# Performance work log

Measured on AMD Instinct MI355X. Metric: run time of the kernel, lower is better.

The kernel has to match this reference:

```python
import jax, jax.numpy as jnp
import numpy as np

EMB = 1024

def setup_inputs() -> dict:
    key = jax.random.key(0)
    ks = jax.random.split(key, 6)
    B, S, E = 4, 2048, EMB
    x = jax.random.normal(ks[0], (B, S, E), dtype=jnp.float32)
    attention_mask = jax.random.randint(ks[1], (B, S, S), 0, 2, dtype=jnp.int32)
    proj_w = jax.random.normal(ks[2], (E, 3 * E), dtype=jnp.float32) * (1.0 / np.sqrt(E))
    proj_b = jax.random.normal(ks[3], (3 * E,), dtype=jnp.float32) * 0.02
    out_w = jax.random.normal(ks[4], (E, E), dtype=jnp.float32) * (1.0 / np.sqrt(E))
    out_b = jax.random.normal(ks[5], (E,), dtype=jnp.float32) * 0.02
    return {"x": x, "attention_mask": attention_mask, "proj_w": proj_w,
            "proj_b": proj_b, "out_w": out_w, "out_b": out_b}

def reference(x, attention_mask, proj_w, proj_b, out_w, out_b):
    E = x.shape[-1]
    scale = 1.0 / jnp.sqrt(jnp.asarray(E, x.dtype))
    qkv = x @ proj_w + proj_b                      # [B,S,3E]
    q, k, v = jnp.split(qkv, 3, axis=-1)           # each [B,S,E]
    scores = jnp.einsum('bqe,bke->bqk', q, k) * scale  # [B,S,S]
    scores = jnp.where(attention_mask == 0, jnp.asarray(-1e20, scores.dtype), scores)
    attn = jax.nn.softmax(scores, axis=-1)
    ctx = jnp.einsum('bqk,bke->bqe', attn, v)      # [B,S,E]
    return ctx @ out_w + out_b
```

## Files before the change

### kernel.cpp

```cpp
#include <hip/hip_runtime.h>
#include <cstdint>

typedef unsigned short u16;
typedef uint32_t u32;
typedef __bf16 bf16x8 __attribute__((ext_vector_type(8)));
typedef float f32x4 __attribute__((ext_vector_type(4)));

__device__ __forceinline__ u16 f2bf(float f) {
  unsigned u = __float_as_uint(f);
  u += 0x7fffu + ((u >> 16) & 1u);
  return (u16)(u >> 16);
}

__device__ __forceinline__ void async16(const void* g, void* l) {
  __builtin_amdgcn_global_load_lds(
      (const __attribute__((address_space(1))) uint32_t*)g,
      (__attribute__((address_space(3))) uint32_t*)l, 16, 0, 0);
}

__global__ __launch_bounds__(256) void k_prep(const float* __restrict__ x, u16* __restrict__ xb,
                                              const float* __restrict__ pw, u16* __restrict__ wt,
                                              const float* __restrict__ ow, u16* __restrict__ owt,
                                              const int* __restrict__ mask, u32* __restrict__ mbits) {
  const int bid = blockIdx.x;
  if (bid < 8192) {
    const int i = bid * 256 + threadIdx.x;
    const float4 v = ((const float4*)x)[i];
    ushort4 o;
    o.x = f2bf(v.x); o.y = f2bf(v.y); o.z = f2bf(v.z); o.w = f2bf(v.w);
    ((ushort4*)xb)[i] = o;
    return;
  }
  if (bid >= 12288) {
    const size_t w = (size_t)(bid - 12288) * 256 + threadIdx.x;
    const int* p = mask + w * 32;
    u32 bits = 0;
#pragma unroll
    for (int j = 0; j < 8; ++j) {
      const int4 v = ((const int4*)p)[j];
      bits |= (u32)(v.x & 1) << (j * 4 + 0);
      bits |= (u32)(v.y & 1) << (j * 4 + 1);
      bits |= (u32)(v.z & 1) << (j * 4 + 2);
      bits |= (u32)(v.w & 1) << (j * 4 + 3);
    }
    mbits[w] = bits;
    return;
  }
  __shared__ u16 tile[32][33];
  const int tx = threadIdx.x & 31, ty = threadIdx.x >> 5;
  const float* in;
  u16* outp;
  int lda, ldo, c0, r0;
  if (bid < 11264) {
    const int id = bid - 8192;
    c0 = (id % 96) * 32; r0 = (id / 96) * 32;
    in = pw; outp = wt; lda = 3072; ldo = 1024;
  } else {
    const int id = bid - 11264;
    c0 = (id % 32) * 32; r0 = (id / 32) * 32;
    in = ow; outp = owt; lda = 1024; ldo = 1024;
  }
#pragma unroll
  for (int i = 0; i < 4; ++i)
    tile[ty + i * 8][tx] = f2bf(in[(size_t)(r0 + ty + i * 8) * lda + c0 + tx]);
  __syncthreads();
#pragma unroll
  for (int i = 0; i < 4; ++i)
    outp[(size_t)(c0 + ty + i * 8) * ldo + r0 + tx] = tile[tx][ty + i * 8];
}

template <int MODE>
__global__ __launch_bounds__(512, 4) void gemm256(
    const u16* __restrict__ A, long lda, long bsA,
    const u16* __restrict__ Bt, long ldb, long bsB,
    void* __restrict__ C, long ldc, long bsC,
    int M, int N, int K,
    const float* __restrict__ bias, const u32* __restrict__ mbits) {
  __shared__ u16 sm[3][12288];
  const int gx = gridDim.x, gxy = gridDim.x * gridDim.y;
  const int T = gxy * gridDim.z;
  int L = blockIdx.x + gx * blockIdx.y + gxy * blockIdx.z;
  L = (L & 7) * (T >> 3) + (L >> 3);
  const int b = L / gxy, rr = L % gxy, bx = rr % gx, by = rr / gx;
  const int m0 = by * 256, n0 = bx * 128;
  const int tid = threadIdx.x;
  const int lane = tid & 63;
  const int w = tid >> 6;
  const int wr = w >> 1, wc = w & 1;

  const int sl = tid >> 3;
  const int sgo = (tid & 7) ^ (sl & 7);
  const int srow = 2 * sl + (sgo >> 2);
  const int skoff = (sgo & 3) * 8;
  const u16* pa = A + (size_t)b * bsA + (size_t)(m0 + srow) * lda + skoff;
  const u16* pb = Bt + (size_t)b * bsB + (size_t)(n0 + srow) * ldb + skoff;
  const size_t a128 = (size_t)128 * lda;

  const int m_l = lane & 15, q = lane >> 4;
  const int l7 = m_l >> 1;
  const int g = (((m_l & 1) * 4) + q) ^ l7;
  const int aoff = wr * 2048 + l7 * 64 + g * 8;
  const int boff = 8192 + wc * 2048 + l7 * 64 + g * 8;

  f32x4 acc[4][4] = {};

#define MFMA_(A_, B_, C_) __builtin_amdgcn_mfma_f32_16x16x32_bf16(A_, B_, C_, 0, 0, 0)
#define STAGE(tt, bi)                               \
  {                                                 \
    const size_t ko_ = (size_t)(tt)*32;             \
    u16* da_ = &sm[bi][0] + tid * 8;                \
    async16(pa + ko_, da_);                         \
    async16(pa + ko_ + a128, da_ + 4096);           \
    async16(pb + ko_, &sm[bi][8192] + tid * 8);     \
  }

  const int NTL = K >> 5;
  STAGE(0, 0) STAGE(1, 1)
  asm volatile("s_waitcnt vmcnt(3)" ::: "memory");
  asm volatile("s_barrier" ::: "memory");

  int br = 0, bs = 2;
  for (int t = 0; t < NTL; ++t) {
    if (t + 2 < NTL) STAGE(t + 2, bs)
    const u16* ab = &sm[br][0] + aoff;
    const u16* bb = &sm[br][0] + boff;
    bf16x8 af[4], bf[4];
#pragma unroll
    for (int mt = 0; mt < 4; ++mt) af[mt] = *(const bf16x8*)(ab + mt * 512);
#pragma unroll
    for (int nt = 0; nt < 4; ++nt) bf[nt] = *(const bf16x8*)(bb + nt * 512);
    __builtin_amdgcn_s_setprio(1);
#pragma unroll
    for (int mt = 0; mt < 4; ++mt)
#pragma unroll
      for (int nt = 0; nt < 4; ++nt)
        acc[mt][nt] = MFMA_(af[mt], bf[nt], acc[mt][nt]);
    __builtin_amdgcn_s_setprio(0);
    if (t + 2 < NTL) {
      asm volatile("s_waitcnt vmcnt(3)" ::: "memory");
    } else if (t + 1 < NTL) {
      asm volatile("s_waitcnt vmcnt(0)" ::: "memory");
    }
    if (t + 1 < NTL) asm volatile("s_barrier" ::: "memory");
    br = (br == 2) ? 0 : br + 1;
    bs = (bs == 2) ? 0 : bs + 1;
  }
#undef STAGE
#undef MFMA_

  if constexpr (MODE == 1) {
    __syncthreads();
    u32* smw = (u32*)&sm[0][0];
    const int rl = tid >> 1, pr = tid & 1;
    const uint2 mv = *(const uint2*)(mbits + ((size_t)b * M + m0 + rl) * (N >> 5) + (n0 >> 5) + pr * 2);
    smw[rl * 4 + pr * 2] = mv.x;
    smw[rl * 4 + pr * 2 + 1] = mv.y;
    __syncthreads();
  }

#pragma unroll
  for (int mt = 0; mt < 4; ++mt) {
#pragma unroll
    for (int nt = 0; nt < 4; ++nt) {
      const int col = n0 + wc * 64 + nt * 16 + m_l;
      const int row0 = m0 + wr * 64 + mt * 16 + q * 4;
#pragma unroll
      for (int r = 0; r < 4; ++r) {
        const int row = row0 + r;
        float v = acc[mt][nt][r];
        if constexpr (MODE == 0) {
          v += bias[col];
          if (col < 1024) v *= 0.03125f;
          ((u16*)C)[(size_t)b * bsC + (size_t)row * ldc + col] = f2bf(v);
        } else {
          const int cl = wc * 64 + nt * 16 + m_l;
          const int rl2 = wr * 64 + mt * 16 + q * 4 + r;
          const u32 wb = ((const u32*)&sm[0][0])[rl2 * 4 + (cl >> 5)];
          v = ((wb >> (cl & 31)) & 1u) ? __expf(fminf(v, 30.f)) : 0.f;
          ((u16*)C)[(size_t)b * bsC + (size_t)row * ldc + col] = f2bf(v);
        }
      }
    }
  }
}

template <int MODE, int TM, int BN>
__device__ __forceinline__ void gemm_core(
    u16* As, u16* Bs,
    const u16* __restrict__ A, long lda, long bsA,
    const u16* __restrict__ Bt, long ldb, long bsB,
    void* __restrict__ C, long ldc, long bsC,
    int M, int N, int K,
    const float* __restrict__ bias, const u32* __restrict__ mbits,
    int b, int bx, int by) {
  constexpr int MT = TM / 32, NT = BN / 32;
  constexpr int ACALLS = TM / 8, TOT = (TM + BN) / 8, NC = TOT / 4;
  const int m0 = by * TM, n0 = bx * BN;
  const int lane = threadIdx.x & 63;
  const int w = threadIdx.x >> 6;
  const int wr = w >> 1, wc = w & 1;

  const int srow = lane >> 3;
  const int scol = ((lane & 7) ^ ((lane >> 3) & 7)) * 8;
  const u16* pa = A + (size_t)b * bsA + (size_t)(m0 + srow) * lda + scol;
  const u16* pb = Bt + (size_t)b * bsB + (size_t)(n0 + srow) * ldb + scol;

  const int m_l = lane & 15, q = lane >> 4, m7 = m_l & 7;
  const int offs[2] = {(q ^ m7) * 8, ((4 + q) ^ m7) * 8};

  f32x4 acc[MT][NT] = {};
  f32x4 accs[MT] = {};
  bf16x8 ones;
#pragma unroll
  for (int e = 0; e < 8; ++e) ones[e] = (__bf16)1.0f;

  for (int kt = 0; kt < K; kt += 64) {
    __syncthreads();
#pragma unroll
    for (int g = 0; g < NC; ++g) {
      const int idx = w * NC + g;
      if (idx < ACALLS)
        async16(pa + (size_t)(idx * 8) * lda, As + idx * 512);
      else
        async16(pb + (size_t)((idx - ACALLS) * 8) * ldb, Bs + (idx - ACALLS) * 512);
    }
    __syncthreads();
#pragma unroll
    for (int s = 0; s < 2; ++s) {
      bf16x8 af[MT], bfr[NT];
#pragma unroll
      for (int t = 0; t < MT; ++t)
        af[t] = *(const bf16x8*)(As + (wr * (TM / 2) + t * 16 + m_l) * 64 + offs[s]);
#pragma unroll
      for (int t = 0; t < NT; ++t)
        bfr[t] = *(const bf16x8*)(Bs + (wc * (BN / 2) + t * 16 + m_l) * 64 + offs[s]);
#pragma unroll
      for (int mt = 0; mt < MT; ++mt)
#pragma unroll
        for (int nt = 0; nt < NT; ++nt)
          acc[mt][nt] = __builtin_amdgcn_mfma_f32_16x16x32_bf16(af[mt], bfr[nt], acc[mt][nt], 0, 0, 0);
      if constexpr (MODE == 2) {
#pragma unroll
        for (int mt = 0; mt < MT; ++mt)
          accs[mt] = __builtin_amdgcn_mfma_f32_16x16x32_bf16(af[mt], ones, accs[mt], 0, 0, 0);
      }
    }
    pa += 64;
    pb += 64;
  }

  float rinv[MT][4];
  if constexpr (MODE == 2) {
#pragma unroll
    for (int mt = 0; mt < MT; ++mt)
#pragma unroll
      for (int r = 0; r < 4; ++r) rinv[mt][r] = 1.0f / accs[mt][r];
  }

#pragma unroll
  for (int mt = 0; mt < MT; ++mt) {
#pragma unroll
    for (int nt = 0; nt < NT; ++nt) {
      const int col = n0 + wc * (BN / 2) + nt * 16 + m_l;
      const int row0 = m0 + wr * (TM / 2) + mt * 16 + q * 4;
      if constexpr (MODE == 3) {
        ushort4 o;
        o.x = f2bf(acc[mt][nt][0]); o.y = f2bf(acc[mt][nt][1]);
        o.z = f2bf(acc[mt][nt][2]); o.w = f2bf(acc[mt][nt][3]);
        *(ushort4*)((u16*)C + (size_t)b * bsC + (size_t)col * ldc + row0) = o;
      } else {
#pragma unroll
        for (int r = 0; r < 4; ++r) {
          const int row = row0 + r;
          float v = acc[mt][nt][r];
          if constexpr (MODE == 2) {
            v = v * rinv[mt][r] + bias[col];
            ((float*)C)[(size_t)b * bsC + (size_t)row * ldc + col] = v;
          }
        }
      }
    }
  }
}

template <int MODE, int TM, int BN>
__global__ __launch_bounds__(256) void gemm_bt(
    const u16* __restrict__ A, long lda, long bsA,
    const u16* __restrict__ Bt, long ldb, long bsB,
    void* __restrict__ C, long ldc, long bsC,
    int M, int N, int K,
    const float* __restrict__ bias, const u32* __restrict__ mbits) {
  __shared__ u16 As[TM * 64];
  __shared__ u16 Bs[BN * 64];
  const int gx = gridDim.x, gxy = gridDim.x * gridDim.y;
  const int T = gxy * gridDim.z;
  int L = blockIdx.x + gx * blockIdx.y + gxy * blockIdx.z;
  L = (L & 7) * (T >> 3) + (L >> 3);
  const int bz = L / gxy, r = L % gxy;
  gemm_core<MODE, TM, BN>(As, Bs, A, lda, bsA, Bt, ldb, bsB, C, ldc, bsC, M, N, K,
                          bias, mbits, bz, r % gx, r / gx);
}

extern "C" void kernel_launch(void* const* d_in, const int* in_sizes, int n_in,
                              void* d_out, int out_size, void* d_ws, size_t ws_size,
                              hipStream_t stream) {
  const float* x = (const float*)d_in[0];
  const int* mask = (const int*)d_in[1];
  const float* proj_w = (const float*)d_in[2];
  const float* proj_b = (const float*)d_in[3];
  const float* out_w = (const float*)d_in[4];
  const float* out_b = (const float*)d_in[5];
  float* out = (float*)d_out;

  char* ws = (char*)d_ws;
  u16* xb = (u16*)(ws);
  u16* wt = (u16*)(ws + 16777216);
  u16* owt = (u16*)(ws + 23068672);
  u16* qkv = (u16*)(ws + 25165824);
  u16* P = (u16*)(ws + 75497472);
  u32* mbits = (u32*)(ws + 109051904);
  u16* Ut = (u16*)xb;

  k_prep<<<14336, 256, 0, stream>>>(x, xb, proj_w, wt, out_w, owt, mask, mbits);
  gemm256<0><<<dim3(24, 32, 1), 512, 0, stream>>>(
      xb, 1024, 0, wt, 1024, 0, qkv, 3072, 0, 8192, 3072, 1024, proj_b, nullptr);
  gemm256<1><<<dim3(16, 8, 4), 512, 0, stream>>>(
      qkv, 3072, (long)2048 * 3072, qkv + 1024, 3072, (long)2048 * 3072,
      P, 2048, (long)2048 * 2048, 2048, 2048, 1024, nullptr, mbits);
  gemm_bt<3, 64, 128><<<dim3(8, 32, 4), 256, 0, stream>>>(
      qkv + 2048, 3072, (long)2048 * 3072, owt, 1024, 0,
      Ut, 2048, (long)1024 * 2048, 2048, 1024, 1024, nullptr, nullptr);
  gemm_bt<2, 128, 128><<<dim3(8, 16, 4), 256, 0, stream>>>(
      P, 2048, (long)2048 * 2048, Ut, 2048, (long)1024 * 2048,
      out, 1024, (long)2048 * 1024, 2048, 1024, 2048, out_b, nullptr);
}
```

Measured before the change: 316.5 us.

## Route V·Wo and P·U GEMMs through the 256-tile triple-buffered kernel

Removes the simpler gemm_bt kernel, which used single-buffered 64/128 tiles. The two remaining GEMMs (V times out_w, and P times U with the row-sum normalisation) now run in the gemm256 kernel, which has 256x128 tiles, 512 threads and a three-stage async global-to-LDS pipeline. The row-sum MFMA against a ones vector and the reciprocal normalisation are moved into gemm256 for MODE 2. The aim is more data reuse per tile and better overlap of loads with MFMA. The cost is far fewer blocks: 256 per GEMM on a GPU with many CUs, which may leave compute units idle.

```diff
diff --git a/kernel.cpp b/kernel.cpp
--- a/kernel.cpp
+++ b/kernel.cpp
@@ -103,6 +103,10 @@
   const int boff = 8192 + wc * 2048 + l7 * 64 + g * 8;
 
   f32x4 acc[4][4] = {};
+  f32x4 accs[4] = {};
+  bf16x8 ones;
+#pragma unroll
+  for (int e = 0; e < 8; ++e) ones[e] = (__bf16)1.0f;
 
 #define MFMA_(A_, B_, C_) __builtin_amdgcn_mfma_f32_16x16x32_bf16(A_, B_, C_, 0, 0, 0)
 #define STAGE(tt, bi)                               \
@@ -135,6 +139,11 @@
 #pragma unroll
       for (int nt = 0; nt < 4; ++nt)
         acc[mt][nt] = MFMA_(af[mt], bf[nt], acc[mt][nt]);
+    if constexpr (MODE == 2) {
+#pragma unroll
+      for (int mt = 0; mt < 4; ++mt)
+        accs[mt] = MFMA_(af[mt], ones, accs[mt]);
+    }
     __builtin_amdgcn_s_setprio(0);
     if (t + 2 < NTL) {
       asm volatile("s_waitcnt vmcnt(3)" ::: "memory");
@@ -158,111 +167,20 @@
     __syncthreads();
   }
 
+  float rinv[4][4];
+  if constexpr (MODE == 2) {
+#pragma unroll
+    for (int mt = 0; mt < 4; ++mt)
+#pragma unroll
+      for (int r = 0; r < 4; ++r) rinv[mt][r] = 1.0f / accs[mt][r];
+  }
+
 #pragma unroll
   for (int mt = 0; mt < 4; ++mt) {
 #pragma unroll
     for (int nt = 0; nt < 4; ++nt) {
       const int col = n0 + wc * 64 + nt * 16 + m_l;
       const int row0 = m0 + wr * 64 + mt * 16 + q * 4;
-#pragma unroll
-      for (int r = 0; r < 4; ++r) {
-        const int row = row0 + r;
-        float v = acc[mt][nt][r];
-        if constexpr (MODE == 0) {
-          v += bias[col];
-          if (col < 1024) v *= 0.03125f;
-          ((u16*)C)[(size_t)b * bsC + (size_t)row * ldc + col] = f2bf(v);
-        } else {
-          const int cl = wc * 64 + nt * 16 + m_l;
-          const int rl2 = wr * 64 + mt * 16 + q * 4 + r;
-          const u32 wb = ((const u32*)&sm[0][0])[rl2 * 4 + (cl >> 5)];
-          v = ((wb >> (cl & 31)) & 1u) ? __expf(fminf(v, 30.f)) : 0.f;
-          ((u16*)C)[(size_t)b * bsC + (size_t)row * ldc + col] = f2bf(v);
-        }
-      }
-    }
-  }
-}
-
-template <int MODE, int TM, int BN>
-__device__ __forceinline__ void gemm_core(
-    u16* As, u16* Bs,
-    const u16* __restrict__ A, long lda, long bsA,
-    const u16* __restrict__ Bt, long ldb, long bsB,
-    void* __restrict__ C, long ldc, long bsC,
-    int M, int N, int K,
-    const float* __restrict__ bias, const u32* __restrict__ mbits,
-    int b, int bx, int by) {
-  constexpr int MT = TM / 32, NT = BN / 32;
-  constexpr int ACALLS = TM / 8, TOT = (TM + BN) / 8, NC = TOT / 4;
-  const int m0 = by * TM, n0 = bx * BN;
-  const int lane = threadIdx.x & 63;
-  const int w = threadIdx.x >> 6;
-  const int wr = w >> 1, wc = w & 1;
-
-  const int srow = lane >> 3;
-  const int scol = ((lane & 7) ^ ((lane >> 3) & 7)) * 8;
-  const u16* pa = A + (size_t)b * bsA + (size_t)(m0 + srow) * lda + scol;
-  const u16* pb = Bt + (size_t)b * bsB + (size_t)(n0 + srow) * ldb + scol;
-
-  const int m_l = lane & 15, q = lane >> 4, m7 = m_l & 7;
-  const int offs[2] = {(q ^ m7) * 8, ((4 + q) ^ m7) * 8};
-
-  f32x4 acc[MT][NT] = {};
-  f32x4 accs[MT] = {};
-  bf16x8 ones;
-#pragma unroll
-  for (int e = 0; e < 8; ++e) ones[e] = (__bf16)1.0f;
-
-  for (int kt = 0; kt < K; kt += 64) {
-    __syncthreads();
-#pragma unroll
-    for (int g = 0; g < NC; ++g) {
-      const int idx = w * NC + g;
-      if (idx < ACALLS)
-        async16(pa + (size_t)(idx * 8) * lda, As + idx * 512);
-      else
-        async16(pb + (size_t)((idx - ACALLS) * 8) * ldb, Bs + (idx - ACALLS) * 512);
-    }
-    __syncthreads();
-#pragma unroll
-    for (int s = 0; s < 2; ++s) {
-      bf16x8 af[MT], bfr[NT];
-#pragma unroll
-      for (int t = 0; t < MT; ++t)
-        af[t] = *(const bf16x8*)(As + (wr * (TM / 2) + t * 16 + m_l) * 64 + offs[s]);
-#pragma unroll
-      for (int t = 0; t < NT; ++t)
-        bfr[t] = *(const bf16x8*)(Bs + (wc * (BN / 2) + t * 16 + m_l) * 64 + offs[s]);
-#pragma unroll
-      for (int mt = 0; mt < MT; ++mt)
-#pragma unroll
-        for (int nt = 0; nt < NT; ++nt)
-          acc[mt][nt] = __builtin_amdgcn_mfma_f32_16x16x32_bf16(af[mt], bfr[nt], acc[mt][nt], 0, 0, 0);
-      if constexpr (MODE == 2) {
-#pragma unroll
-        for (int mt = 0; mt < MT; ++mt)
-          accs[mt] = __builtin_amdgcn_mfma_f32_16x16x32_bf16(af[mt], ones, accs[mt], 0, 0, 0);
-      }
-    }
-    pa += 64;
-    pb += 64;
-  }
-
-  float rinv[MT][4];
-  if constexpr (MODE == 2) {
-#pragma unroll
-    for (int mt = 0; mt < MT; ++mt)
-#pragma unroll
-      for (int r = 0; r < 4; ++r) rinv[mt][r] = 1.0f / accs[mt][r];
-  }
-
-#pragma unroll
-  for (int mt = 0; mt < MT; ++mt) {
-#pragma unroll
-    for (int nt = 0; nt < NT; ++nt) {
-      const int col = n0 + wc * (BN / 2) + nt * 16 + m_l;
-      const int row0 = m0 + wr * (TM / 2) + mt * 16 + q * 4;
       if constexpr (MODE == 3) {
         ushort4 o;
         o.x = f2bf(acc[mt][nt][0]); o.y = f2bf(acc[mt][nt][1]);
@@ -273,7 +191,17 @@
         for (int r = 0; r < 4; ++r) {
           const int row = row0 + r;
           float v = acc[mt][nt][r];
-          if constexpr (MODE == 2) {
+          if constexpr (MODE == 0) {
+            v += bias[col];
+            if (col < 1024) v *= 0.03125f;
+            ((u16*)C)[(size_t)b * bsC + (size_t)row * ldc + col] = f2bf(v);
+          } else if constexpr (MODE == 1) {
+            const int cl = wc * 64 + nt * 16 + m_l;
+            const int rl2 = wr * 64 + mt * 16 + q * 4 + r;
+            const u32 wb = ((const u32*)&sm[0][0])[rl2 * 4 + (cl >> 5)];
+            v = ((wb >> (cl & 31)) & 1u) ? __expf(fminf(v, 30.f)) : 0.f;
+            ((u16*)C)[(size_t)b * bsC + (size_t)row * ldc + col] = f2bf(v);
+          } else if constexpr (MODE == 2) {
             v = v * rinv[mt][r] + bias[col];
             ((float*)C)[(size_t)b * bsC + (size_t)row * ldc + col] = v;
           }
@@ -281,24 +209,6 @@
       }
     }
   }
-}
-
-template <int MODE, int TM, int BN>
-__global__ __launch_bounds__(256) void gemm_bt(
-    const u16* __restrict__ A, long lda, long bsA,
-    const u16* __restrict__ Bt, long ldb, long bsB,
-    void* __restrict__ C, long ldc, long bsC,
-    int M, int N, int K,
-    const float* __restrict__ bias, const u32* __restrict__ mbits) {
-  __shared__ u16 As[TM * 64];
-  __shared__ u16 Bs[BN * 64];
-  const int gx = gridDim.x, gxy = gridDim.x * gridDim.y;
-  const int T = gxy * gridDim.z;
-  int L = blockIdx.x + gx * blockIdx.y + gxy * blockIdx.z;
-  L = (L & 7) * (T >> 3) + (L >> 3);
-  const int bz = L / gxy, r = L % gxy;
-  gemm_core<MODE, TM, BN>(As, Bs, A, lda, bsA, Bt, ldb, bsB, C, ldc, bsC, M, N, K,
-                          bias, mbits, bz, r % gx, r / gx);
 }
 
 extern "C" void kernel_launch(void* const* d_in, const int* in_sizes, int n_in,
@@ -327,10 +237,10 @@
   gemm256<1><<<dim3(16, 8, 4), 512, 0, stream>>>(
       qkv, 3072, (long)2048 * 3072, qkv + 1024, 3072, (long)2048 * 3072,
       P, 2048, (long)2048 * 2048, 2048, 2048, 1024, nullptr, mbits);
-  gemm_bt<3, 64, 128><<<dim3(8, 32, 4), 256, 0, stream>>>(
+  gemm256<3><<<dim3(8, 8, 4), 512, 0, stream>>>(
       qkv + 2048, 3072, (long)2048 * 3072, owt, 1024, 0,
       Ut, 2048, (long)1024 * 2048, 2048, 1024, 1024, nullptr, nullptr);
-  gemm_bt<2, 128, 128><<<dim3(8, 16, 4), 256, 0, stream>>>(
+  gemm256<2><<<dim3(8, 8, 4), 512, 0, stream>>>(
       P, 2048, (long)2048 * 2048, Ut, 2048, (long)1024 * 2048,
       out, 1024, (long)2048 * 1024, 2048, 1024, 2048, out_b, nullptr);
 }
```

Measured after the change: 319.9 us. Within noise of the previous version (+1.1%).
